# Performance work log

Measured on AMD Instinct MI355X. Metric: run time of the kernel, lower is better.

## Reference

```python
import jax, jax.numpy as jnp
import numpy as np
from jax import lax

D_MODEL = 1024
D_STATE = 128
D_CONV = 4
EXPAND = 2
HEADDIM = 64
D_INNER = EXPAND * D_MODEL          # 2048
NHEADS = D_INNER // HEADDIM          # 32
CONV_DIM = D_INNER + 2 * D_STATE     # 2304
D_IN_PROJ = 2 * D_INNER + 2 * D_STATE + NHEADS  # 4384
B_SZ, L_SEQ = 4, 2048
EPS = 1e-5


def setup_inputs() -> dict:
    key = jax.random.key(0)
    ks = jax.random.split(key, 10)
    x = jax.random.normal(ks[0], (B_SZ, L_SEQ, D_MODEL), dtype=jnp.float32)
    in_proj_w = jax.random.normal(ks[1], (D_IN_PROJ, D_MODEL), dtype=jnp.float32) * 0.02
    conv_w = jax.random.normal(ks[2], (CONV_DIM, D_CONV), dtype=jnp.float32) * 0.2
    conv_b = jax.random.normal(ks[3], (CONV_DIM,), dtype=jnp.float32) * 0.02
    dt_bias = jax.random.normal(ks[4], (NHEADS,), dtype=jnp.float32) * 0.5
    A_log = jnp.log(jax.random.uniform(ks[5], (NHEADS,), minval=1.0, maxval=16.0, dtype=jnp.float32))
    D = 1.0 + 0.1 * jax.random.normal(ks[6], (NHEADS,), dtype=jnp.float32)
    norm_w = jnp.ones((D_INNER,), dtype=jnp.float32)
    out_proj_w = jax.random.normal(ks[7], (D_MODEL, D_INNER), dtype=jnp.float32) * 0.02
    ln_w = jnp.ones((D_MODEL,), dtype=jnp.float32)
    ln_b = jnp.zeros((D_MODEL,), dtype=jnp.float32)
    return {"x": x, "in_proj_w": in_proj_w, "conv_w": conv_w, "conv_b": conv_b,
            "dt_bias": dt_bias, "A_log": A_log, "D": D, "norm_w": norm_w,
            "out_proj_w": out_proj_w, "ln_w": ln_w, "ln_b": ln_b}


def _mamba_block(x, in_proj_w, conv_w, conv_b, dt_bias, A_log, D, norm_w, out_proj_w, ln_w, ln_b):
    b, l, _ = x.shape
    # 1. input projection -> z, xBC, dt
    zxbcdt = jnp.einsum('bld,ed->ble', x, in_proj_w)  # (b,l,D_IN_PROJ)
    z = zxbcdt[..., :D_INNER]
    xBC = zxbcdt[..., D_INNER:D_INNER + CONV_DIM]
    dt = jax.nn.softplus(zxbcdt[..., D_INNER + CONV_DIM:] + dt_bias)  # (b,l,H)
    # 2. causal depthwise conv1d + silu
    xBC_t = xBC.transpose(0, 2, 1)  # (b,CONV_DIM,l)
    conv = lax.conv_general_dilated(xBC_t, conv_w[:, None, :], (1,), [(D_CONV - 1, 0)],
                                    feature_group_count=CONV_DIM,
                                    dimension_numbers=('NCW', 'OIW', 'NCW'))
    xBC = jax.nn.silu(conv + conv_b[:, None]).transpose(0, 2, 1)  # (b,l,CONV_DIM)
    x_ssm = xBC[..., :D_INNER].reshape(b, l, NHEADS, HEADDIM)     # (b,l,h,p)
    Bm = xBC[..., D_INNER:D_INNER + D_STATE]                      # (b,l,n) ngroups=1
    Cm = xBC[..., D_INNER + D_STATE:]                             # (b,l,n)
    # 3. selective scan
    A = -jnp.exp(A_log)               # (h,)
    dA = jnp.exp(dt * A)              # (b,l,h)
    def step(h, inp):
        dA_t, x_t, B_t, C_t, dt_t = inp  # (b,h),(b,h,p),(b,n),(b,n),(b,h)
        dBx = dt_t[:, :, None, None] * x_t[..., None] * B_t[:, None, None, :]
        h = h * dA_t[:, :, None, None] + dBx                       # (b,h,p,n)
        y = jnp.einsum('bhpn,bn->bhp', h, C_t)
        return h, y
    h0 = jnp.zeros((b, NHEADS, HEADDIM, D_STATE), dtype=x.dtype)
    inputs = (dA.transpose(1, 0, 2), x_ssm.transpose(1, 0, 2, 3),
              Bm.transpose(1, 0, 2), Cm.transpose(1, 0, 2), dt.transpose(1, 0, 2))
    _, ys = lax.scan(step, h0, inputs)                             # (l,b,h,p)
    y = ys.transpose(1, 0, 2, 3) + D[None, None, :, None] * x_ssm  # skip D term
    y = y.reshape(b, l, D_INNER)
    # 4. gated RMSNorm (norm_before_gate=False): gate first, then normalize
    y = y * jax.nn.silu(z)
    y = y * lax.rsqrt(jnp.mean(y * y, axis=-1, keepdims=True) + EPS) * norm_w
    # 5. output projection + residual
    y = jnp.einsum('bld,ed->ble', y, out_proj_w) + x
    # 6. LayerNorm (dropout is identity in eval)
    mu = jnp.mean(y, axis=-1, keepdims=True)
    var = jnp.mean((y - mu) ** 2, axis=-1, keepdims=True)
    return (y - mu) * lax.rsqrt(var + EPS) * ln_w + ln_b


def reference(x, in_proj_w, conv_w, conv_b, dt_bias, A_log, D, norm_w, out_proj_w, ln_w, ln_b):
    return _mamba_block(x, in_proj_w, conv_w, conv_b, dt_bias, A_log, D, norm_w, out_proj_w, ln_w, ln_b)
```

## Files before the change

### kernel.cpp

```cpp
#include <hip/hip_runtime.h>

typedef unsigned short u16;
typedef unsigned int   u32;

#define L_SEQ    2048
#define D_MODEL  1024
#define D_STATE  128
#define D_INNER  2048
#define NHEADS   32
#define HEADDIM  64
#define CONV_DIM 2304
#define D_IN_PROJ 4384
#define EPSF     1e-5f
#define QC       128
#define NCH      16

using frag  = __attribute__((ext_vector_type(8))) short;
using f32x4 = __attribute__((ext_vector_type(4))) float;
typedef __attribute__((ext_vector_type(8))) unsigned short u16x8;

__device__ __forceinline__ u16 f2bf(float f) {
  u32 u = __float_as_uint(f);
  return (u16)((u + 0x7fffu + ((u >> 16) & 1u)) >> 16);
}
__device__ __forceinline__ float bf2f(u16 u) {
  return __uint_as_float(((u32)u) << 16);
}
__device__ __forceinline__ void async16(const void* g, void* l) {
  __builtin_amdgcn_global_load_lds((const __attribute__((address_space(1))) u32*)g,
                                   (__attribute__((address_space(3))) u32*)l, 16, 0, 0);
}

__global__ __launch_bounds__(256) void k_cvt_all(const float* __restrict__ x,
                                                 u16* __restrict__ xb,
                                                 const float* __restrict__ w1,
                                                 u16* __restrict__ w1b,
                                                 const float* __restrict__ w2,
                                                 u16* __restrict__ w2b) {
  int bid = blockIdx.x;
  int t = threadIdx.x;
  const float* src;
  u16* dst;
  int i;
  if (bid < 8192)       { i = bid * 256 + t;          src = x;  dst = xb;  }
  else if (bid < 12576) { i = (bid - 8192) * 256 + t; src = w1; dst = w1b; }
  else if (bid < 14624) { i = (bid - 12576) * 256 + t; src = w2; dst = w2b; }
  else {
    i = (bid - 14624) * 256 + t;
    ((ushort4*)(w1b + (size_t)4384 * 1024))[i] = ushort4{0, 0, 0, 0};
    return;
  }
  float4 v = ((const float4*)src)[i];
  ushort4 o;
  o.x = f2bf(v.x); o.y = f2bf(v.y); o.z = f2bf(v.z); o.w = f2bf(v.w);
  ((ushort4*)dst)[i] = o;
}

template <int MODE>
__global__ __launch_bounds__(256) void k_gemm(const u16* __restrict__ A,
                                              const u16* __restrict__ B, int K,
                                              int Nvalid, int ldc,
                                              u16* __restrict__ Cb,
                                              float* __restrict__ Cf,
                                              const float* __restrict__ resid,
                                              float* __restrict__ Cdt) {
  __shared__ __attribute__((aligned(16))) u16 As[2][128 * 32];
  __shared__ __attribute__((aligned(16))) u16 Bs[2][128 * 32];
  const int tid = threadIdx.x;
  const int lane = tid & 63;
  const int wid = tid >> 6;
  const int wm = wid >> 1, wn = wid & 1;
  const int m0 = blockIdx.x * 128, n0 = blockIdx.y * 128;

  f32x4 acc[4][4];
#pragma unroll
  for (int i = 0; i < 4; ++i)
#pragma unroll
    for (int j = 0; j < 4; ++j) acc[i][j] = f32x4{0.f, 0.f, 0.f, 0.f};

  const char* gA[2]; const char* gB[2];
  int cbo[2];
#pragma unroll
  for (int j = 0; j < 2; ++j) {
    int base = (wid * 2 + j) * 1024;
    int p = base + lane * 16;
    int row = p >> 6;
    int colb = p & 63;
    gA[j] = (const char*)A + ((size_t)(m0 + row) * K) * 2 + colb;
    gB[j] = (const char*)B + ((size_t)(n0 + row) * K) * 2 + colb;
    cbo[j] = base;
  }

#define STAGE(bufi, kt) do { size_t kb = (size_t)(kt) * 64; \
    async16(gA[0] + kb, (char*)As[bufi] + cbo[0]); \
    async16(gA[1] + kb, (char*)As[bufi] + cbo[1]); \
    async16(gB[0] + kb, (char*)Bs[bufi] + cbo[0]); \
    async16(gB[1] + kb, (char*)Bs[bufi] + cbo[1]); } while (0)

  const int kg = (lane >> 4) * 16;
  const int rr = wm * 64 + (lane & 15);
  const int cc = wn * 64 + (lane & 15);

  STAGE(0, 0);
  const int nt = K >> 5;
  for (int t = 0; t < nt; ++t) {
    const int cur = t & 1;
    if (t + 1 < nt) {
      STAGE(cur ^ 1, t + 1);
      asm volatile("s_waitcnt vmcnt(4)" ::: "memory");
    } else {
      asm volatile("s_waitcnt vmcnt(0)" ::: "memory");
    }
    asm volatile("s_barrier" ::: "memory");
    frag af[4], bfr[4];
#pragma unroll
    for (int mi = 0; mi < 4; ++mi)
      af[mi] = *(const frag*)((const char*)As[cur] + (rr + mi * 16) * 64 + kg);
#pragma unroll
    for (int ni = 0; ni < 4; ++ni)
      bfr[ni] = *(const frag*)((const char*)Bs[cur] + (cc + ni * 16) * 64 + kg);
#pragma unroll
    for (int mi = 0; mi < 4; ++mi)
#pragma unroll
      for (int ni = 0; ni < 4; ++ni)
        acc[mi][ni] = __builtin_amdgcn_mfma_f32_16x16x32_bf16(af[mi], bfr[ni],
                                                              acc[mi][ni], 0, 0, 0);
    asm volatile("s_waitcnt lgkmcnt(0)" ::: "memory");
    asm volatile("s_barrier" ::: "memory");
  }
#undef STAGE

  const int er = (lane >> 4) * 4;
  const int ec = lane & 15;
#pragma unroll
  for (int mi = 0; mi < 4; ++mi) {
#pragma unroll
    for (int ni = 0; ni < 4; ++ni) {
      int col = n0 + wn * 64 + ni * 16 + ec;
      if (col < Nvalid) {
#pragma unroll
        for (int r = 0; r < 4; ++r) {
          int row = m0 + wm * 64 + mi * 16 + er + r;
          size_t off = (size_t)row * ldc + col;
          float v = acc[mi][ni][r];
          if (MODE == 1) {
            Cb[off] = f2bf(v);
            if (col >= D_INNER + CONV_DIM)
              Cdt[(size_t)row * NHEADS + (col - D_INNER - CONV_DIM)] = v;
          } else {
            Cf[off] = v + resid[off];
          }
        }
      }
    }
  }
}

__global__ __launch_bounds__(256) void k_convcum(const u16* __restrict__ zxb,
                                                 const float* __restrict__ cw,
                                                 const float* __restrict__ cb,
                                                 u16* __restrict__ xcb,
                                                 u16* __restrict__ bcb,
                                                 const float* __restrict__ dtf,
                                                 const float* __restrict__ dtb,
                                                 const float* __restrict__ alog,
                                                 float* __restrict__ dtv,
                                                 float* __restrict__ cumv) {
  int bid = blockIdx.x;
  if (bid < 2048) {
    int b = bid >> 9;
    int l0 = (bid & 511) * 4;
    size_t rowbase = (size_t)b * L_SEQ + l0;
    for (int g = threadIdx.x; g < CONV_DIM / 4; g += 256) {
      int c = g * 4;
      float4 w0 = ((const float4*)cw)[c + 0];
      float4 w1 = ((const float4*)cw)[c + 1];
      float4 w2 = ((const float4*)cw)[c + 2];
      float4 w3 = ((const float4*)cw)[c + 3];
      float4 bias = *(const float4*)(cb + c);
      ushort4 xv[7];
#pragma unroll
      for (int k = 0; k < 7; ++k) {
        int lm = l0 - 3 + k;
        xv[k] = (lm >= 0)
            ? *(const ushort4*)(zxb + (rowbase + (k - 3)) * D_IN_PROJ + D_INNER + c)
            : ushort4{0, 0, 0, 0};
      }
#pragma unroll
      for (int dl = 0; dl < 4; ++dl) {
        float a0 = bias.x, a1 = bias.y, a2 = bias.z, a3 = bias.w;
#pragma unroll
        for (int k = 0; k < 4; ++k) {
          ushort4 v = xv[dl + k];
          a0 = fmaf(bf2f(v.x), (&w0.x)[k], a0);
          a1 = fmaf(bf2f(v.y), (&w1.x)[k], a1);
          a2 = fmaf(bf2f(v.z), (&w2.x)[k], a2);
          a3 = fmaf(bf2f(v.w), (&w3.x)[k], a3);
        }
        a0 = a0 / (1.f + __expf(-a0));
        a1 = a1 / (1.f + __expf(-a1));
        a2 = a2 / (1.f + __expf(-a2));
        a3 = a3 / (1.f + __expf(-a3));
        ushort4 o;
        o.x = f2bf(a0); o.y = f2bf(a1); o.z = f2bf(a2); o.w = f2bf(a3);
        size_t row = rowbase + dl;
        if (c < D_INNER) {
          *(ushort4*)(xcb + row * D_INNER + c) = o;
        } else {
          *(ushort4*)(bcb + row * 256 + (c - D_INNER)) = o;
        }
      }
    }
    return;
  }
  int cb_ = bid - 2048;
  int c = cb_ & (NCH - 1);
  int bh = cb_ >> 4;
  int h = bh & 31, b = bh >> 5;
  int t = threadIdx.x;
  float x = 0.f, dt = 0.f;
  if (t < 128) {
    int l = c * QC + t;
    float raw = dtf[((size_t)(b * L_SEQ + l)) * NHEADS + h] + dtb[h];
    dt = raw > 20.f ? raw : log1pf(expf(raw));
    float A = -expf(alog[h]);
    x = dt * A;
    int lane = t & 63;
#pragma unroll
    for (int off = 1; off < 64; off <<= 1) {
      float up = __shfl_up(x, off);
      if (lane >= off) x += up;
    }
  }
  __shared__ float wtot;
  if (t == 63) wtot = x;
  __syncthreads();
  if (t < 128) {
    if (t >= 64) x += wtot;
    size_t o = (size_t)bh * L_SEQ + c * QC + t;
    dtv[o] = dt;
    cumv[o] = x;
  }
}

__global__ __launch_bounds__(256) void k_ssd1(const u16* __restrict__ xcb,
                                              const u16* __restrict__ bcb,
                                              const float* __restrict__ dtv,
                                              const float* __restrict__ cumv,
                                              u16* __restrict__ SH,
                                              u16* __restrict__ Gb) {
  __shared__ __attribute__((aligned(16))) char smem[52736];
  int bid = blockIdx.x;
  int tid = threadIdx.x, lane = tid & 63, wid = tid >> 6;
  int wm = wid >> 1, wn = wid & 1;
  const int er = (lane >> 4) * 4;
  const int ec = lane & 15;

  if (bid < 2048) {
    u16* XT = (u16*)smem;
    u16* BW = (u16*)(smem + 17408);
    float* wlds = (float*)(smem + 52224);
    int c = bid & (NCH - 1);
    int bh = bid >> 4;
    int h = bh & 31, b = bh >> 5;
    int l0 = c * QC;
    size_t bhl = (size_t)bh * L_SEQ + l0;
    if (tid < 128) {
      float ce = cumv[bhl + 127];
      wlds[tid] = __expf(ce - cumv[bhl + tid]) * dtv[bhl + tid];
    }
    const int jrow = tid & 127;
    const u16* xbase = xcb + ((size_t)(b * L_SEQ + l0)) * D_INNER + h * HEADDIM;
    {
      int sb = (tid >> 7) * 4;
#pragma unroll
      for (int s = 0; s < 4; ++s) {
        int seg = sb + s;
        u16x8 xv = *(const u16x8*)(xbase + (size_t)jrow * D_INNER + seg * 8);
#pragma unroll
        for (int k = 0; k < 8; ++k) XT[(seg * 8 + k) * 136 + jrow] = xv[k];
      }
    }
    __syncthreads();
    const u16* bbase = bcb + (size_t)(b * L_SEQ + l0) * 256;
    {
      int sb = (tid >> 7) * 8;
      float w = wlds[jrow];
#pragma unroll
      for (int s = 0; s < 8; ++s) {
        int seg = sb + s;
        u16x8 bv = *(const u16x8*)(bbase + (size_t)jrow * 256 + seg * 8);
#pragma unroll
        for (int k = 0; k < 8; ++k)
          BW[(seg * 8 + k) * 136 + jrow] = f2bf(bf2f(bv[k]) * w);
      }
    }
    __syncthreads();
    f32x4 acc[2][4];
#pragma unroll
    for (int i = 0; i < 2; ++i)
#pragma unroll
      for (int j = 0; j < 4; ++j) acc[i][j] = f32x4{0.f, 0.f, 0.f, 0.f};
    int rr = wm * 32 + (lane & 15);
    int cc = wn * 64 + (lane & 15);
#pragma unroll
    for (int kk = 0; kk < 4; ++kk) {
      int ko = kk * 32 + (lane >> 4) * 8;
      frag af[2], bfr[4];
#pragma unroll
      for (int mi = 0; mi < 2; ++mi)
        af[mi] = *(const frag*)&XT[(rr + mi * 16) * 136 + ko];
#pragma unroll
      for (int ni = 0; ni < 4; ++ni)
        bfr[ni] = *(const frag*)&BW[(cc + ni * 16) * 136 + ko];
#pragma unroll
      for (int mi = 0; mi < 2; ++mi)
#pragma unroll
        for (int ni = 0; ni < 4; ++ni)
          acc[mi][ni] = __builtin_amdgcn_mfma_f32_16x16x32_bf16(af[mi], bfr[ni],
                                                                acc[mi][ni], 0, 0, 0);
    }
    u16* sbase = SH + ((size_t)(bh * NCH + c)) * (64 * 128);
#pragma unroll
    for (int mi = 0; mi < 2; ++mi)
#pragma unroll
      for (int ni = 0; ni < 4; ++ni)
#pragma unroll
        for (int r = 0; r < 4; ++r) {
          int p = wm * 32 + mi * 16 + er + r;
          int n = wn * 64 + ni * 16 + ec;
          sbase[(size_t)p * 128 + n] = f2bf(acc[mi][ni][r]);
        }
  } else {
    u16* Cs = (u16*)smem;
    u16* Bs = (u16*)(smem + 17408);
    int gbid = bid - 2048;
    int half = gbid & 1;
    int c = (gbid >> 1) & (NCH - 1);
    int b = gbid >> 5;
    const u16* base = bcb + (size_t)(b * L_SEQ + c * QC) * 256;
    for (int idx = tid; idx < 128 * 16; idx += 256) {
      int j = idx >> 4, seg = idx & 15;
      *(u16x8*)&Bs[j * 136 + seg * 8] = *(const u16x8*)(base + (size_t)j * 256 + seg * 8);
    }
    for (int idx = tid; idx < 64 * 16; idx += 256) {
      int i = idx >> 4, seg = idx & 15;
      *(u16x8*)&Cs[i * 136 + seg * 8] =
          *(const u16x8*)(base + (size_t)(half * 64 + i) * 256 + 128 + seg * 8);
    }
    __syncthreads();
    f32x4 acc[2][4];
#pragma unroll
    for (int i = 0; i < 2; ++i)
#pragma unroll
      for (int j = 0; j < 4; ++j) acc[i][j] = f32x4{0.f, 0.f, 0.f, 0.f};
    int rr = wm * 32 + (lane & 15);
    int cc = wn * 64 + (lane & 15);
#pragma unroll
    for (int kk = 0; kk < 4; ++kk) {
      int ko = kk * 32 + (lane >> 4) * 8;
      frag af[2], bfr[4];
#pragma unroll
      for (int mi = 0; mi < 2; ++mi)
        af[mi] = *(const frag*)&Cs[(rr + mi * 16) * 136 + ko];
#pragma unroll
      for (int ni = 0; ni < 4; ++ni)
        bfr[ni] = *(const frag*)&Bs[(cc + ni * 16) * 136 + ko];
#pragma unroll
      for (int mi = 0; mi < 2; ++mi)
#pragma unroll
        for (int ni = 0; ni < 4; ++ni)
          acc[mi][ni] = __builtin_amdgcn_mfma_f32_16x16x32_bf16(af[mi], bfr[ni],
                                                                acc[mi][ni], 0, 0, 0);
    }
    u16* gbase = Gb + ((size_t)(b * NCH + c)) * 128 * 128;
#pragma unroll
    for (int mi = 0; mi < 2; ++mi)
#pragma unroll
      for (int ni = 0; ni < 4; ++ni)
#pragma unroll
        for (int r = 0; r < 4; ++r) {
          int i = half * 64 + wm * 32 + mi * 16 + er + r;
          int j = wn * 64 + ni * 16 + ec;
          gbase[(size_t)i * 128 + j] = f2bf(acc[mi][ni][r]);
        }
  }
}

__global__ __launch_bounds__(512) void k_chain(u16* __restrict__ SH,
                                               const float* __restrict__ cumv) {
  int bid = blockIdx.x;
  int half = bid & 1;
  int bh = bid >> 1;
  int t = threadIdx.x;
  u16* base = SH + (size_t)bh * NCH * 8192 + half * 4096 + t * 8;
  float H[8];
#pragma unroll
  for (int i = 0; i < 8; ++i) H[i] = 0.f;
  u16x8 s = *(const u16x8*)base;
  float e = __expf(cumv[(size_t)bh * L_SEQ + 127]);
  for (int c = 0; c < NCH; ++c) {
    u16x8 cs = s;
    float ce = e;
    if (c + 1 < NCH) {
      s = *(const u16x8*)(base + (size_t)(c + 1) * 8192);
      e = __expf(cumv[(size_t)bh * L_SEQ + (c + 1) * QC + 127]);
    }
    u16x8 h0;
#pragma unroll
    for (int k = 0; k < 8; ++k) h0[k] = f2bf(H[k]);
    *(u16x8*)(base + (size_t)c * 8192) = h0;
#pragma unroll
    for (int k = 0; k < 8; ++k) H[k] = fmaf(H[k], ce, bf2f(cs[k]));
  }
}

__global__ __launch_bounds__(256) void k_y(const u16* __restrict__ xcb,
                                           const u16* __restrict__ bcb,
                                           const float* __restrict__ dtv,
                                           const float* __restrict__ cumv,
                                           const u16* __restrict__ Gb,
                                           const u16* __restrict__ SH,
                                           u16* __restrict__ ysb) {
  __shared__ u16 Abuf[128 * 136];
  __shared__ u16 Bbuf[64 * 136];
  __shared__ float cums[128], dts[128];
  int bid = blockIdx.x;
  int c = bid & (NCH - 1);
  int bh = bid >> 4;
  int h = bh & 31, b = bh >> 5;
  int tid = threadIdx.x, lane = tid & 63, wid = tid >> 6;
  int wm = wid >> 1, wn = wid & 1;
  int l0 = c * QC;
  size_t bhl = (size_t)bh * L_SEQ + l0;
  if (tid < 128) { cums[tid] = cumv[bhl + tid]; dts[tid] = dtv[bhl + tid]; }
  const u16* xbase = xcb + ((size_t)(b * L_SEQ + l0)) * D_INNER + h * HEADDIM;
  {
    int jrow = tid & 127;
    int sb = (tid >> 7) * 4;
#pragma unroll
    for (int s = 0; s < 4; ++s) {
      int seg = sb + s;
      u16x8 xv = *(const u16x8*)(xbase + (size_t)jrow * D_INNER + seg * 8);
#pragma unroll
      for (int k = 0; k < 8; ++k) Bbuf[(seg * 8 + k) * 136 + jrow] = xv[k];
    }
  }
  __syncthreads();
  const u16* gbase = Gb + ((size_t)(b * NCH + c)) * 128 * 128;
  for (int idx = tid; idx < 128 * 16; idx += 256) {
    int i = idx >> 4, seg = idx & 15;
    int j0 = seg * 8;
    u16x8 o;
    if (j0 > i) {
#pragma unroll
      for (int k = 0; k < 8; ++k) o[k] = 0;
    } else {
      u16x8 g = *(const u16x8*)(gbase + (size_t)i * 128 + j0);
      float ci = cums[i];
#pragma unroll
      for (int k = 0; k < 8; ++k) {
        int j = j0 + k;
        float m = (j <= i) ? bf2f(g[k]) * __expf(ci - cums[j]) * dts[j] : 0.f;
        o[k] = f2bf(m);
      }
    }
    *(u16x8*)&Abuf[i * 136 + j0] = o;
  }
  __syncthreads();
  f32x4 acc1[4][2], acc2[4][2];
#pragma unroll
  for (int i = 0; i < 4; ++i)
#pragma unroll
    for (int j = 0; j < 2; ++j) {
      acc1[i][j] = f32x4{0.f, 0.f, 0.f, 0.f};
      acc2[i][j] = f32x4{0.f, 0.f, 0.f, 0.f};
    }
  int rr = wm * 64 + (lane & 15);
  int cc = wn * 32 + (lane & 15);
#pragma unroll
  for (int kk = 0; kk < 4; ++kk) {
    int ko = kk * 32 + (lane >> 4) * 8;
    frag af[4], bfr[2];
#pragma unroll
    for (int mi = 0; mi < 4; ++mi)
      af[mi] = *(const frag*)&Abuf[(rr + mi * 16) * 136 + ko];
#pragma unroll
    for (int ni = 0; ni < 2; ++ni)
      bfr[ni] = *(const frag*)&Bbuf[(cc + ni * 16) * 136 + ko];
#pragma unroll
    for (int mi = 0; mi < 4; ++mi)
#pragma unroll
      for (int ni = 0; ni < 2; ++ni)
        acc1[mi][ni] = __builtin_amdgcn_mfma_f32_16x16x32_bf16(af[mi], bfr[ni],
                                                               acc1[mi][ni], 0, 0, 0);
  }
  __syncthreads();
  const u16* cbase = bcb + (size_t)(b * L_SEQ + l0) * 256 + 128;
  for (int idx = tid; idx < 128 * 16; idx += 256) {
    int i = idx >> 4, seg = idx & 15;
    *(u16x8*)&Abuf[i * 136 + seg * 8] = *(const u16x8*)(cbase + (size_t)i * 256 + seg * 8);
  }
  const u16* hbase = SH + ((size_t)(bh * NCH + c)) * (64 * 128);
  for (int idx = tid; idx < 64 * 16; idx += 256) {
    int p = idx >> 4, seg = idx & 15;
    *(u16x8*)&Bbuf[p * 136 + seg * 8] = *(const u16x8*)(hbase + (size_t)p * 128 + seg * 8);
  }
  __syncthreads();
#pragma unroll
  for (int kk = 0; kk < 4; ++kk) {
    int ko = kk * 32 + (lane >> 4) * 8;
    frag af[4], bfr[2];
#pragma unroll
    for (int mi = 0; mi < 4; ++mi)
      af[mi] = *(const frag*)&Abuf[(rr + mi * 16) * 136 + ko];
#pragma unroll
    for (int ni = 0; ni < 2; ++ni)
      bfr[ni] = *(const frag*)&Bbuf[(cc + ni * 16) * 136 + ko];
#pragma unroll
    for (int mi = 0; mi < 4; ++mi)
#pragma unroll
      for (int ni = 0; ni < 2; ++ni)
        acc2[mi][ni] = __builtin_amdgcn_mfma_f32_16x16x32_bf16(af[mi], bfr[ni],
                                                               acc2[mi][ni], 0, 0, 0);
  }
  const int er = (lane >> 4) * 4;
  const int ec = lane & 15;
#pragma unroll
  for (int mi = 0; mi < 4; ++mi)
#pragma unroll
    for (int r = 0; r < 4; ++r) {
      int i = wm * 64 + mi * 16 + er + r;
      float e = __expf(cums[i]);
#pragma unroll
      for (int ni = 0; ni < 2; ++ni) {
        int p = wn * 32 + ni * 16 + ec;
        float v = acc1[mi][ni][r] + e * acc2[mi][ni][r];
        ysb[((size_t)(b * L_SEQ + l0 + i)) * D_INNER + h * HEADDIM + p] = f2bf(v);
      }
    }
}

__global__ __launch_bounds__(256) void k_gate(const u16* __restrict__ ysb,
                                              const u16* __restrict__ xcb,
                                              const u16* __restrict__ zxb,
                                              const float* __restrict__ Dp,
                                              const float* __restrict__ nw,
                                              u16* __restrict__ yb) {
  int row = blockIdx.x;
  int t = threadIdx.x;
  int d0 = t * 8;
  float Dh = Dp[d0 >> 6];
  u16x8 ya = *(const u16x8*)(ysb + (size_t)row * D_INNER + d0);
  u16x8 xa = *(const u16x8*)(xcb + (size_t)row * D_INNER + d0);
  u16x8 za = *(const u16x8*)(zxb + (size_t)row * D_IN_PROJ + d0);
  float v[8];
  float ss = 0.f;
#pragma unroll
  for (int c = 0; c < 8; ++c) {
    float val = bf2f(ya[c]) + Dh * bf2f(xa[c]);
    float zz = bf2f(za[c]);
    val *= zz / (1.f + __expf(-zz));
    v[c] = val;
    ss += val * val;
  }
  __shared__ float red[4];
#pragma unroll
  for (int off = 32; off; off >>= 1) ss += __shfl_xor(ss, off);
  if ((t & 63) == 0) red[t >> 6] = ss;
  __syncthreads();
  float tot = red[0] + red[1] + red[2] + red[3];
  float scale = rsqrtf(tot * (1.f / D_INNER) + EPSF);
  float4 w0 = *(const float4*)(nw + d0);
  float4 w1 = *(const float4*)(nw + d0 + 4);
  u16x8 o;
  o[0] = f2bf(v[0] * scale * w0.x);
  o[1] = f2bf(v[1] * scale * w0.y);
  o[2] = f2bf(v[2] * scale * w0.z);
  o[3] = f2bf(v[3] * scale * w0.w);
  o[4] = f2bf(v[4] * scale * w1.x);
  o[5] = f2bf(v[5] * scale * w1.y);
  o[6] = f2bf(v[6] * scale * w1.z);
  o[7] = f2bf(v[7] * scale * w1.w);
  *(u16x8*)(yb + (size_t)row * D_INNER + d0) = o;
}

union F4 { float4 v; float f[4]; };
__global__ __launch_bounds__(256) void k_ln(float* __restrict__ io,
                                            const float* __restrict__ lw,
                                            const float* __restrict__ lb) {
  int row = blockIdx.x;
  int t = threadIdx.x;
  int d0 = t * 4;
  F4 v; v.v = *(const float4*)(io + (size_t)row * D_MODEL + d0);
  float s1 = v.f[0] + v.f[1] + v.f[2] + v.f[3];
  float s2 = v.f[0] * v.f[0] + v.f[1] * v.f[1] + v.f[2] * v.f[2] + v.f[3] * v.f[3];
  __shared__ float r1[4], r2[4];
#pragma unroll
  for (int off = 32; off; off >>= 1) {
    s1 += __shfl_xor(s1, off);
    s2 += __shfl_xor(s2, off);
  }
  if ((t & 63) == 0) { r1[t >> 6] = s1; r2[t >> 6] = s2; }
  __syncthreads();
  float S1 = r1[0] + r1[1] + r1[2] + r1[3];
  float S2 = r2[0] + r2[1] + r2[2] + r2[3];
  float mu = S1 * (1.f / D_MODEL);
  float var = S2 * (1.f / D_MODEL) - mu * mu;
  float inv = rsqrtf(var + EPSF);
  F4 w, bb, o;
  w.v = *(const float4*)(lw + d0);
  bb.v = *(const float4*)(lb + d0);
#pragma unroll
  for (int c = 0; c < 4; ++c) o.f[c] = (v.f[c] - mu) * inv * w.f[c] + bb.f[c];
  *(float4*)(io + (size_t)row * D_MODEL + d0) = o.v;
}

extern "C" void kernel_launch(void* const* d_in, const int* in_sizes, int n_in,
                              void* d_out, int out_size, void* d_ws, size_t ws_size,
                              hipStream_t stream) {
  const float* x    = (const float*)d_in[0];
  const float* w1   = (const float*)d_in[1];
  const float* cw   = (const float*)d_in[2];
  const float* cb   = (const float*)d_in[3];
  const float* dtb  = (const float*)d_in[4];
  const float* alog = (const float*)d_in[5];
  const float* Dp   = (const float*)d_in[6];
  const float* nw   = (const float*)d_in[7];
  const float* w2   = (const float*)d_in[8];
  const float* lw   = (const float*)d_in[9];
  const float* lb   = (const float*)d_in[10];
  float* out = (float*)d_out;
  char* ws = (char*)d_ws;

  u16*   xb   = (u16*)(ws + 0);
  u16*   w1b  = (u16*)(ws + 16777216);
  u16*   w2b  = (u16*)(ws + 25952256);
  u16*   zxb  = (u16*)(ws + 30146560);
  u16*   xcb  = (u16*)(ws + 101974016);
  float* dtf  = (float*)(ws + 135528448);
  float* dtv  = (float*)(ws + 136577024);
  float* cumv = (float*)(ws + 137625600);
  u16*   ysb  = (u16*)(ws + 138674176);
  u16*   yb   = (u16*)(ws + 172228608);
  u16*   Gb   = (u16*)(ws + 205783040);
  if (ws_size < (size_t)209977344) return;

  u16* bcb = (u16*)out;
  u16* SH  = yb;

  k_cvt_all<<<14720, 256, 0, stream>>>(x, xb, w1, w1b, w2, w2b);

  k_gemm<1><<<dim3(64, 35), 256, 0, stream>>>(xb, w1b, 1024, 4384, 4384,
                                              zxb, nullptr, nullptr, dtf);

  k_convcum<<<4096, 256, 0, stream>>>(zxb, cw, cb, xcb, bcb, dtf, dtb, alog, dtv, cumv);

  k_ssd1<<<2048 + 128, 256, 0, stream>>>(xcb, bcb, dtv, cumv, SH, Gb);
  k_chain<<<256, 512, 0, stream>>>(SH, cumv);
  k_y<<<128 * NCH, 256, 0, stream>>>(xcb, bcb, dtv, cumv, Gb, SH, ysb);

  k_gate<<<8192, 256, 0, stream>>>(ysb, xcb, zxb, Dp, nw, yb);

  k_gemm<0><<<dim3(64, 8), 256, 0, stream>>>(yb, w2b, 2048, 1024, 1024,
                                             nullptr, out, x, nullptr);

  k_ln<<<8192, 256, 0, stream>>>(out, lw, lb);
}
```

Baseline: 300.5 us.

## Fuse gated RMSNorm into SSD output kernel and out-projection epilogue

New measurement: 300.9 us. Within noise of the previous version (+0.1%).

```diff
diff --git a/kernel.cpp b/kernel.cpp
--- a/kernel.cpp
+++ b/kernel.cpp
@@ -36,15 +36,25 @@
                                                  const float* __restrict__ w1,
                                                  u16* __restrict__ w1b,
                                                  const float* __restrict__ w2,
-                                                 u16* __restrict__ w2b) {
+                                                 u16* __restrict__ w2b,
+                                                 const float* __restrict__ nw) {
   int bid = blockIdx.x;
   int t = threadIdx.x;
+  if (bid >= 12576 && bid < 14624) {
+    int i = (bid - 12576) * 256 + t;
+    float4 v = ((const float4*)w2)[i];
+    float4 wv = *(const float4*)(nw + ((i * 4) & (D_INNER - 1)));
+    ushort4 o;
+    o.x = f2bf(v.x * wv.x); o.y = f2bf(v.y * wv.y);
+    o.z = f2bf(v.z * wv.z); o.w = f2bf(v.w * wv.w);
+    ((ushort4*)w2b)[i] = o;
+    return;
+  }
   const float* src;
   u16* dst;
   int i;
   if (bid < 8192)       { i = bid * 256 + t;          src = x;  dst = xb;  }
   else if (bid < 12576) { i = (bid - 8192) * 256 + t; src = w1; dst = w1b; }
-  else if (bid < 14624) { i = (bid - 12576) * 256 + t; src = w2; dst = w2b; }
   else {
     i = (bid - 14624) * 256 + t;
     ((ushort4*)(w1b + (size_t)4384 * 1024))[i] = ushort4{0, 0, 0, 0};
@@ -63,7 +73,8 @@
                                               u16* __restrict__ Cb,
                                               float* __restrict__ Cf,
                                               const float* __restrict__ resid,
-                                              float* __restrict__ Cdt) {
+                                              float* __restrict__ Cdt,
+                                              const float* __restrict__ sumsq) {
   __shared__ __attribute__((aligned(16))) u16 As[2][128 * 32];
   __shared__ __attribute__((aligned(16))) u16 Bs[2][128 * 32];
   const int tid = threadIdx.x;
@@ -132,24 +143,37 @@
 
   const int er = (lane >> 4) * 4;
   const int ec = lane & 15;
-#pragma unroll
-  for (int mi = 0; mi < 4; ++mi) {
-#pragma unroll
-    for (int ni = 0; ni < 4; ++ni) {
-      int col = n0 + wn * 64 + ni * 16 + ec;
-      if (col < Nvalid) {
-#pragma unroll
-        for (int r = 0; r < 4; ++r) {
-          int row = m0 + wm * 64 + mi * 16 + er + r;
-          size_t off = (size_t)row * ldc + col;
-          float v = acc[mi][ni][r];
-          if (MODE == 1) {
+  if (MODE == 1) {
+#pragma unroll
+    for (int mi = 0; mi < 4; ++mi) {
+#pragma unroll
+      for (int ni = 0; ni < 4; ++ni) {
+        int col = n0 + wn * 64 + ni * 16 + ec;
+        if (col < Nvalid) {
+#pragma unroll
+          for (int r = 0; r < 4; ++r) {
+            int row = m0 + wm * 64 + mi * 16 + er + r;
+            size_t off = (size_t)row * ldc + col;
+            float v = acc[mi][ni][r];
             Cb[off] = f2bf(v);
             if (col >= D_INNER + CONV_DIM)
               Cdt[(size_t)row * NHEADS + (col - D_INNER - CONV_DIM)] = v;
-          } else {
-            Cf[off] = v + resid[off];
           }
+        }
+      }
+    }
+  } else {
+#pragma unroll
+    for (int mi = 0; mi < 4; ++mi) {
+#pragma unroll
+      for (int r = 0; r < 4; ++r) {
+        int row = m0 + wm * 64 + mi * 16 + er + r;
+        float sc = rsqrtf(sumsq[row] * (1.f / D_INNER) + EPSF);
+#pragma unroll
+        for (int ni = 0; ni < 4; ++ni) {
+          int col = n0 + wn * 64 + ni * 16 + ec;
+          size_t off = (size_t)row * ldc + col;
+          Cf[off] = acc[mi][ni][r] * sc + resid[off];
         }
       }
     }
@@ -248,7 +272,8 @@
                                               const float* __restrict__ dtv,
                                               const float* __restrict__ cumv,
                                               u16* __restrict__ SH,
-                                              u16* __restrict__ Gb) {
+                                              u16* __restrict__ Gb,
+                                              float* __restrict__ sumsq) {
   __shared__ __attribute__((aligned(16))) char smem[52736];
   int bid = blockIdx.x;
   int tid = threadIdx.x, lane = tid & 63, wid = tid >> 6;
@@ -335,6 +360,7 @@
     u16* Cs = (u16*)smem;
     u16* Bs = (u16*)(smem + 17408);
     int gbid = bid - 2048;
+    if (gbid < 32) sumsq[gbid * 256 + tid] = 0.f;
     int half = gbid & 1;
     int c = (gbid >> 1) & (NCH - 1);
     int b = gbid >> 5;
@@ -417,14 +443,18 @@
 
 __global__ __launch_bounds__(256) void k_y(const u16* __restrict__ xcb,
                                            const u16* __restrict__ bcb,
+                                           const u16* __restrict__ zxb,
                                            const float* __restrict__ dtv,
                                            const float* __restrict__ cumv,
                                            const u16* __restrict__ Gb,
                                            const u16* __restrict__ SH,
-                                           u16* __restrict__ ysb) {
+                                           const float* __restrict__ Dp,
+                                           u16* __restrict__ ysb,
+                                           float* __restrict__ sumsq) {
   __shared__ u16 Abuf[128 * 136];
   __shared__ u16 Bbuf[64 * 136];
   __shared__ float cums[128], dts[128];
+  float* rowsq = dts;
   int bid = blockIdx.x;
   int c = bid & (NCH - 1);
   int bh = bid >> 4;
@@ -507,6 +537,7 @@
     *(u16x8*)&Bbuf[p * 136 + seg * 8] = *(const u16x8*)(hbase + (size_t)p * 128 + seg * 8);
   }
   __syncthreads();
+  if (tid < 128) rowsq[tid] = 0.f;
 #pragma unroll
   for (int kk = 0; kk < 4; ++kk) {
     int ko = kk * 32 + (lane >> 4) * 8;
@@ -524,65 +555,36 @@
         acc2[mi][ni] = __builtin_amdgcn_mfma_f32_16x16x32_bf16(af[mi], bfr[ni],
                                                                acc2[mi][ni], 0, 0, 0);
   }
+  __syncthreads();
   const int er = (lane >> 4) * 4;
   const int ec = lane & 15;
+  const float Dh = Dp[h];
 #pragma unroll
   for (int mi = 0; mi < 4; ++mi)
 #pragma unroll
     for (int r = 0; r < 4; ++r) {
       int i = wm * 64 + mi * 16 + er + r;
+      size_t grow = (size_t)(b * L_SEQ + l0 + i);
       float e = __expf(cums[i]);
+      float part = 0.f;
 #pragma unroll
       for (int ni = 0; ni < 2; ++ni) {
         int p = wn * 32 + ni * 16 + ec;
-        float v = acc1[mi][ni][r] + e * acc2[mi][ni][r];
-        ysb[((size_t)(b * L_SEQ + l0 + i)) * D_INNER + h * HEADDIM + p] = f2bf(v);
-      }
-    }
-}
-
-__global__ __launch_bounds__(256) void k_gate(const u16* __restrict__ ysb,
-                                              const u16* __restrict__ xcb,
-                                              const u16* __restrict__ zxb,
-                                              const float* __restrict__ Dp,
-                                              const float* __restrict__ nw,
-                                              u16* __restrict__ yb) {
-  int row = blockIdx.x;
-  int t = threadIdx.x;
-  int d0 = t * 8;
-  float Dh = Dp[d0 >> 6];
-  u16x8 ya = *(const u16x8*)(ysb + (size_t)row * D_INNER + d0);
-  u16x8 xa = *(const u16x8*)(xcb + (size_t)row * D_INNER + d0);
-  u16x8 za = *(const u16x8*)(zxb + (size_t)row * D_IN_PROJ + d0);
-  float v[8];
-  float ss = 0.f;
-#pragma unroll
-  for (int c = 0; c < 8; ++c) {
-    float val = bf2f(ya[c]) + Dh * bf2f(xa[c]);
-    float zz = bf2f(za[c]);
-    val *= zz / (1.f + __expf(-zz));
-    v[c] = val;
-    ss += val * val;
-  }
-  __shared__ float red[4];
-#pragma unroll
-  for (int off = 32; off; off >>= 1) ss += __shfl_xor(ss, off);
-  if ((t & 63) == 0) red[t >> 6] = ss;
-  __syncthreads();
-  float tot = red[0] + red[1] + red[2] + red[3];
-  float scale = rsqrtf(tot * (1.f / D_INNER) + EPSF);
-  float4 w0 = *(const float4*)(nw + d0);
-  float4 w1 = *(const float4*)(nw + d0 + 4);
-  u16x8 o;
-  o[0] = f2bf(v[0] * scale * w0.x);
-  o[1] = f2bf(v[1] * scale * w0.y);
-  o[2] = f2bf(v[2] * scale * w0.z);
-  o[3] = f2bf(v[3] * scale * w0.w);
-  o[4] = f2bf(v[4] * scale * w1.x);
-  o[5] = f2bf(v[5] * scale * w1.y);
-  o[6] = f2bf(v[6] * scale * w1.z);
-  o[7] = f2bf(v[7] * scale * w1.w);
-  *(u16x8*)(yb + (size_t)row * D_INNER + d0) = o;
+        float acc = acc1[mi][ni][r] + e * acc2[mi][ni][r];
+        float xv = bf2f(xcb[grow * D_INNER + h * HEADDIM + p]);
+        float zz = bf2f(zxb[grow * D_IN_PROJ + h * HEADDIM + p]);
+        float val = (acc + Dh * xv) * (zz / (1.f + __expf(-zz)));
+        ysb[grow * D_INNER + h * HEADDIM + p] = f2bf(val);
+        part += val * val;
+      }
+      part += __shfl_xor(part, 1);
+      part += __shfl_xor(part, 2);
+      part += __shfl_xor(part, 4);
+      part += __shfl_xor(part, 8);
+      if ((lane & 15) == 0) atomicAdd(&rowsq[i], part);
+    }
+  __syncthreads();
+  if (tid < 128) atomicAdd(&sumsq[(size_t)b * L_SEQ + l0 + tid], rowsq[tid]);
 }
 
 union F4 { float4 v; float f[4]; };
@@ -648,22 +650,21 @@
 
   u16* bcb = (u16*)out;
   u16* SH  = yb;
-
-  k_cvt_all<<<14720, 256, 0, stream>>>(x, xb, w1, w1b, w2, w2b);
+  float* sumsq = dtf;
+
+  k_cvt_all<<<14720, 256, 0, stream>>>(x, xb, w1, w1b, w2, w2b, nw);
 
   k_gemm<1><<<dim3(64, 35), 256, 0, stream>>>(xb, w1b, 1024, 4384, 4384,
-                                              zxb, nullptr, nullptr, dtf);
+                                              zxb, nullptr, nullptr, dtf, nullptr);
 
   k_convcum<<<4096, 256, 0, stream>>>(zxb, cw, cb, xcb, bcb, dtf, dtb, alog, dtv, cumv);
 
-  k_ssd1<<<2048 + 128, 256, 0, stream>>>(xcb, bcb, dtv, cumv, SH, Gb);
+  k_ssd1<<<2048 + 128, 256, 0, stream>>>(xcb, bcb, dtv, cumv, SH, Gb, sumsq);
   k_chain<<<256, 512, 0, stream>>>(SH, cumv);
-  k_y<<<128 * NCH, 256, 0, stream>>>(xcb, bcb, dtv, cumv, Gb, SH, ysb);
-
-  k_gate<<<8192, 256, 0, stream>>>(ysb, xcb, zxb, Dp, nw, yb);
-
-  k_gemm<0><<<dim3(64, 8), 256, 0, stream>>>(yb, w2b, 2048, 1024, 1024,
-                                             nullptr, out, x, nullptr);
+  k_y<<<128 * NCH, 256, 0, stream>>>(xcb, bcb, zxb, dtv, cumv, Gb, SH, Dp, ysb, sumsq);
+
+  k_gemm<0><<<dim3(64, 8), 256, 0, stream>>>(ysb, w2b, 2048, 1024, 1024,
+                                             nullptr, out, x, nullptr, sumsq);
 
   k_ln<<<8192, 256, 0, stream>>>(out, lw, lb);
 }
```
